# Kernel tuning notes

Hardware: AMD Instinct MI355X
Metric: run time of the kernel (lower is better)

Reference implementation:

```python
import jax, jax.numpy as jnp
import numpy as np

B, S, D, H = 4, 2048, 1024, 16
HD = D // H

def setup_inputs() -> dict:
    key = jax.random.key(0)
    ks = jax.random.split(key, 5)
    x = jax.random.normal(ks[0], (B, S, D), dtype=jnp.float32)
    mask = jnp.ones((B, S), dtype=jnp.int32)
    # torch nn.Linear init scale ~ 1/sqrt(fan_in); use small normal for stability
    qkv_w = jax.random.normal(ks[1], (3 * D, D), dtype=jnp.float32) * (1.0 / np.sqrt(D))
    qkv_b = jax.random.normal(ks[2], (3 * D,), dtype=jnp.float32) * 0.02
    out_w = jax.random.normal(ks[3], (D, D), dtype=jnp.float32) * (1.0 / np.sqrt(D))
    out_b = jax.random.normal(ks[4], (D,), dtype=jnp.float32) * 0.02
    return {"x": x, "mask": mask, "qkv_w": qkv_w, "qkv_b": qkv_b,
            "out_w": out_w, "out_b": out_b}

def reference(x, mask, qkv_w, qkv_b, out_w, out_b):
    b, s, d = x.shape
    scale = np.sqrt(HD).astype(np.float32)
    # qkv projection: torch Linear y = x @ W^T + b
    qkv = x @ qkv_w.T + qkv_b                      # (b, s, 3d)
    qkv = qkv.reshape(b, s, 3, H, HD)
    qkv = jnp.transpose(qkv, (2, 0, 3, 1, 4))      # (3, b, H, s, hd)
    q, k, v = qkv[0], qkv[1], qkv[2]
    scores = jnp.einsum('bhqd,bhkd->bhqk', q, k) / scale  # (b, H, s, s)
    neg_inf = jnp.float32(-jnp.inf)
    causal = jnp.tril(jnp.ones((s, s), dtype=bool))
    scores = jnp.where(causal[None, None], scores, neg_inf)
    key_mask = (mask != 0)[:, None, None, :]       # (b, 1, 1, s)
    scores = jnp.where(key_mask, scores, neg_inf)
    attn = jax.nn.softmax(scores, axis=-1)
    out = jnp.einsum('bhqk,bhkd->bhqd', attn, v)   # (b, H, s, hd)
    out = jnp.transpose(out, (0, 2, 1, 3)).reshape(b, s, d)
    return out @ out_w.T + out_b
```

## Files before the change

kernel.cpp:

```cpp
#include <hip/hip_runtime.h>
#include <stdint.h>
#include <type_traits>

#define BB  4
#define SS  2048
#define DD  1024
#define HH  16
#define HDD 64

typedef __attribute__((ext_vector_type(8)))  short s16x8;
typedef __attribute__((ext_vector_type(4)))  float f32x4;
typedef __attribute__((ext_vector_type(16))) float f32x16;

__device__ inline short f2bf(float f) {
    union { float f; unsigned int u; } v; v.f = f;
    unsigned int r = (v.u + 0x7fffu + ((v.u >> 16) & 1u)) >> 16;
    return (short)r;
}
__device__ inline unsigned int permpack(float a, float b) {
    union { float f; unsigned int u; } x, y; x.f = a; y.f = b;
    return __builtin_amdgcn_perm(y.u + 0x8000u, x.u + 0x8000u, 0x07060302u);
}

#define GLL(gp, lp) __builtin_amdgcn_global_load_lds( \
    (const __attribute__((address_space(1))) void*)(gp), \
    (__attribute__((address_space(3))) void*)(lp), 16, 0, 0)

__global__ void cvt_kernel(const float* __restrict__ src, short* __restrict__ dst, int n) {
    int i = (blockIdx.x * 256 + threadIdx.x) * 8;
    if (i >= n) return;
    const float4* s = (const float4*)(src + i);
    float4 a = s[0], b = s[1];
    s16x8 o;
    o[0]=f2bf(a.x); o[1]=f2bf(a.y); o[2]=f2bf(a.z); o[3]=f2bf(a.w);
    o[4]=f2bf(b.x); o[5]=f2bf(b.y); o[6]=f2bf(b.z); o[7]=f2bf(b.w);
    *(s16x8*)(dst + i) = o;
}

template<int EPI>
__global__ __launch_bounds__(256)
void gemm_bt(const short* __restrict__ A, const short* __restrict__ Bw,
             const float* __restrict__ bias, float* __restrict__ Cf,
             short* __restrict__ Qo, short* __restrict__ Ko, short* __restrict__ Vo,
             int M, int N, int K)
{
    __shared__ short lsA[128 * 32];
    __shared__ short lsB[128 * 32];
    const int tid  = threadIdx.x;
    const int w    = tid >> 6, lane = tid & 63;
    const int quad = lane >> 4, l15 = lane & 15;
    const int m0 = blockIdx.x * 128, n0 = blockIdx.y * 128;
    const int mw = (w & 1) * 64, nw = (w >> 1) * 64;

    f32x4 acc[4][4] = {};

    const int srow = w * 32 + (lane >> 2);
    const int scol = (lane & 3) * 8;
    const short* pA = A + (size_t)(m0 + srow) * K + scol;
    const short* pB = Bw + (size_t)(n0 + srow) * K + scol;
    short* lAbase0 = &lsA[(w * 32) * 32];
    short* lAbase1 = &lsA[(w * 32 + 16) * 32];
    short* lBbase0 = &lsB[(w * 32) * 32];
    short* lBbase1 = &lsB[(w * 32 + 16) * 32];

    for (int kk = 0; kk < K; kk += 32) {
        __syncthreads();
        GLL(pA + kk,            lAbase0);
        GLL(pA + kk + 16 * K,   lAbase1);
        GLL(pB + kk,            lBbase0);
        GLL(pB + kk + 16 * K,   lBbase1);
        asm volatile("s_waitcnt vmcnt(0)" ::: "memory");
        __syncthreads();

        s16x8 af[4], bfr[4];
        for (int t = 0; t < 4; ++t) {
            af[t]  = *(const s16x8*)&lsA[(mw + t * 16 + l15) * 32 + quad * 8];
            bfr[t] = *(const s16x8*)&lsB[(nw + t * 16 + l15) * 32 + quad * 8];
        }
        for (int i = 0; i < 4; ++i)
            for (int j = 0; j < 4; ++j)
                acc[i][j] = __builtin_amdgcn_mfma_f32_16x16x32_bf16(af[i], bfr[j], acc[i][j], 0, 0, 0);
    }

    if (EPI == 0) {
        for (int i = 0; i < 4; ++i) {
            int row = m0 + mw + i * 16 + quad * 4;
            for (int j = 0; j < 4; ++j) {
                int col = n0 + nw + j * 16 + l15;
                float bv = bias[col];
                for (int r = 0; r < 4; ++r)
                    Cf[(size_t)(row + r) * N + col] = acc[i][j][r] + bv;
            }
        }
    } else {
        for (int i = 0; i < 4; ++i) {
            int row = m0 + mw + i * 16 + quad * 4;
            for (int j = 0; j < 4; ++j) {
                int col = n0 + nw + j * 16 + l15;
                float bv = bias[col];
                int sel = col >> 10, h = (col >> 6) & 15, hd = col & 63;
                for (int r = 0; r < 4; ++r) {
                    int rr = row + r;
                    int b = rr >> 11, s = rr & 2047;
                    short val = f2bf(acc[i][j][r] + bv);
                    if (sel == 0)      Qo[(((size_t)b * HH + h) * SS + s) * HDD + hd] = val;
                    else if (sel == 1) Ko[(((size_t)b * HH + h) * SS + s) * HDD + hd] = val;
                    else               Vo[(((size_t)b * HH + h) * HDD + hd) * SS + s] = val;
                }
            }
        }
    }
}

__global__ __launch_bounds__(256, 4)
void attn_kernel(const short* __restrict__ Q, const short* __restrict__ Kb,
                 const short* __restrict__ Vb, const int* __restrict__ mask,
                 short* __restrict__ O)
{
    __shared__ short lsK[2][64 * 64];
    __shared__ short lsV[2][64 * 64];
    __shared__ float lsM[2][64];

    const int tid = threadIdx.x;
    const int w   = tid >> 6, lane = tid & 63;
    const int h   = lane >> 5, q = lane & 31;
    const int bx = blockIdx.x, bh = blockIdx.y;
    const int qb = (bx & 1) ? (15 - (bx >> 1)) : (bx >> 1);
    const int b = bh >> 4;
    const size_t baseQK = (size_t)bh * SS * HDD;
    const size_t baseV  = (size_t)bh * HDD * SS;
    const int q0 = qb * 128;
    const int s_row = q0 + w * 32 + q;
    const int T = 2 * (qb + 1);
    const float SC = 0.18033688f;

    s16x8 bq[4];
    for (int kb = 0; kb < 4; ++kb)
        bq[kb] = *(const s16x8*)(Q + baseQK + (size_t)s_row * HDD + kb * 16 + h * 8);

    const short* gK[2]; const short* gV[2]; int lofs[2];
    for (int i = 0; i < 2; ++i) {
        const int p = w * 128 + i * 64 + lane;
        const int kr = p >> 3, s = p & 7;
        gK[i] = Kb + baseQK + (size_t)kr * HDD + ((s ^ (kr & 7)) * 8);
        gV[i] = Vb + baseV + (size_t)kr * SS + ((s ^ (kr & 7)) * 8);
        lofs[i] = (w * 128 + i * 64) * 8;
    }
    const int* mbase = mask + b * SS;

    float lsum = 0.f;
    f32x16 oa[2] = {};

    for (int i = 0; i < 2; ++i) {
        GLL(gK[i], &lsK[0][lofs[i]]);
        GLL(gV[i], &lsV[0][lofs[i]]);
    }
    if (tid < 16) {
        int4 mv = *(const int4*)(mbase + tid * 4);
        float4 f;
        f.x = mv.x ? 0.f : -1e30f; f.y = mv.y ? 0.f : -1e30f;
        f.z = mv.z ? 0.f : -1e30f; f.w = mv.w ? 0.f : -1e30f;
        *(float4*)&lsM[0][tid * 4] = f;
    }
    __syncthreads();

    auto step = [&](int kt, auto CC) {
        constexpr bool CAUS = decltype(CC)::value;
        const int cur = kt & 1, nxt = cur ^ 1;
        const int kv0 = kt * 64;

        int4 mv;
        const bool pf = (kt + 1 < T);
        if (pf) {
            const size_t okK = (size_t)(kv0 + 64) * HDD;
            const int   okV = kv0 + 64;
            for (int i = 0; i < 2; ++i) {
                GLL(gK[i] + okK, &lsK[nxt][lofs[i]]);
                GLL(gV[i] + okV, &lsV[nxt][lofs[i]]);
            }
            if (tid < 16) mv = *(const int4*)(mbase + kv0 + 64 + tid * 4);
        }

        for (int nt = 0; nt < 2; ++nt) {
            f32x16 sa = {};
            const int key = nt * 32 + q;
            for (int kb = 0; kb < 4; ++kb) {
                const int cc = (kb * 2 + h) ^ (key & 7);
                s16x8 ak = *(const s16x8*)&lsK[cur][(key * 8 + cc) * 8];
                sa = __builtin_amdgcn_mfma_f32_32x32x16_bf16(ak, bq[kb], sa, 0, 0, 0);
            }
            unsigned int pk2[4][2];
            for (int g = 0; g < 4; ++g) {
                float4 mq = *(const float4*)&lsM[cur][nt * 32 + 8 * g + 4 * h];
                float pv[4];
                for (int r = 0; r < 4; ++r) {
                    float v = sa[g * 4 + r] * SC + ((const float*)&mq)[r];
                    if (CAUS) {
                        int keyg = kv0 + nt * 32 + 8 * g + 4 * h + r;
                        if (keyg > s_row) v = -1e30f;
                    }
                    float p = __builtin_amdgcn_exp2f(v);
                    pv[r] = p;
                    lsum += p;
                }
                pk2[g][0] = permpack(pv[0], pv[1]);
                pk2[g][1] = permpack(pv[2], pv[3]);
            }
            for (int kb2 = 0; kb2 < 2; ++kb2) {
                const int g_own = 2 * kb2 + h;
                unsigned int s0 = h ? pk2[2 * kb2][0] : pk2[2 * kb2 + 1][0];
                unsigned int s1 = h ? pk2[2 * kb2][1] : pk2[2 * kb2 + 1][1];
                unsigned int r0 = (unsigned int)__shfl_xor((int)s0, 32);
                unsigned int r1 = (unsigned int)__shfl_xor((int)s1, 32);
                union { s16x8 v; unsigned int d[4]; } bp;
                if (h == 0) { bp.d[0] = pk2[g_own][0]; bp.d[1] = pk2[g_own][1]; bp.d[2] = r0; bp.d[3] = r1; }
                else        { bp.d[0] = r0; bp.d[1] = r1; bp.d[2] = pk2[g_own][0]; bp.d[3] = pk2[g_own][1]; }
                for (int mt = 0; mt < 2; ++mt) {
                    const int hd = mt * 32 + q;
                    const int cc = (nt * 4 + kb2 * 2 + h) ^ (hd & 7);
                    s16x8 av = *(const s16x8*)&lsV[cur][(hd * 8 + cc) * 8];
                    oa[mt] = __builtin_amdgcn_mfma_f32_32x32x16_bf16(av, bp.v, oa[mt], 0, 0, 0);
                }
            }
        }

        if (pf && tid < 16) {
            float4 f;
            f.x = mv.x ? 0.f : -1e30f; f.y = mv.y ? 0.f : -1e30f;
            f.z = mv.z ? 0.f : -1e30f; f.w = mv.w ? 0.f : -1e30f;
            *(float4*)&lsM[nxt][tid * 4] = f;
        }
        __syncthreads();
    };

    int kt = 0;
    for (; kt < T - 2; ++kt) step(kt, std::false_type{});
    step(kt, std::true_type{}); ++kt;
    step(kt, std::true_type{});

    float ls2 = lsum + __shfl_xor(lsum, 32);
    float inv = 1.0f / ls2;
    const int hcol = (bh & 15) * HDD;
    const size_t obase = ((size_t)b * SS + s_row) * DD + hcol;
    for (int mt = 0; mt < 2; ++mt) {
        for (int g = 0; g < 4; ++g) {
            const int hd0 = mt * 32 + 8 * g + 4 * h;
            uint2 st;
            st.x = permpack(oa[mt][g * 4 + 0] * inv, oa[mt][g * 4 + 1] * inv);
            st.y = permpack(oa[mt][g * 4 + 2] * inv, oa[mt][g * 4 + 3] * inv);
            *(uint2*)&O[obase + hd0] = st;
        }
    }
}

extern "C" void kernel_launch(void* const* d_in, const int* in_sizes, int n_in,
                              void* d_out, int out_size, void* d_ws, size_t ws_size,
                              hipStream_t stream) {
    const float* x     = (const float*)d_in[0];
    const int*   mask  = (const int*)d_in[1];
    const float* qkv_w = (const float*)d_in[2];
    const float* qkv_b = (const float*)d_in[3];
    const float* out_w = (const float*)d_in[4];
    const float* out_b = (const float*)d_in[5];
    float* out = (float*)d_out;

    const size_t M1 = (size_t)BB * SS;
    short* ws  = (short*)d_ws;
    short* xb  = ws;
    short* qwb = xb  + M1 * DD;
    short* owb = qwb + (size_t)3 * DD * DD;
    short* Qb  = owb + (size_t)DD * DD;
    short* Kb  = Qb  + M1 * DD;
    short* Vb  = Kb  + M1 * DD;
    short* Ob  = Vb  + M1 * DD;

    cvt_kernel<<<(int)(M1 * DD / 8 / 256), 256, 0, stream>>>(x, xb, (int)(M1 * DD));
    cvt_kernel<<<3 * DD * DD / 8 / 256, 256, 0, stream>>>(qkv_w, qwb, 3 * DD * DD);
    cvt_kernel<<<DD * DD / 8 / 256, 256, 0, stream>>>(out_w, owb, DD * DD);

    gemm_bt<1><<<dim3(64, 24), 256, 0, stream>>>(xb, qwb, qkv_b, nullptr,
                                                 Qb, Kb, Vb, 8192, 3072, 1024);
    attn_kernel<<<dim3(16, BB * HH), 256, 0, stream>>>(Qb, Kb, Vb, mask, Ob);
    gemm_bt<0><<<dim3(64, 8), 256, 0, stream>>>(Ob, owb, out_b, out,
                                                nullptr, nullptr, nullptr, 8192, 1024, 1024);
}
```

Measured before the change: 341.3 us.

## Split attention work across warps by key half and head-dim half per 32-query block

Each attention block now handles only 32 query rows instead of 128. Its four waves split the 64-key tile into two key halves and the head dimension into two halves, and the partial outputs and row sums are combined through shared memory at the end. The grid grows from 16 to 64 blocks per head, with descending query-block order, to improve load balance and occupancy under the causal mask. In exchange, each wave now computes QK^T scores that its partner wave duplicates for the other head-dim half. K/V tiles are also loaded once per 32 queries rather than once per 128, which adds global and LDS traffic.

```diff
diff --git a/kernel.cpp b/kernel.cpp
--- a/kernel.cpp
+++ b/kernel.cpp
@@ -124,14 +124,14 @@
     const int tid = threadIdx.x;
     const int w   = tid >> 6, lane = tid & 63;
     const int h   = lane >> 5, q = lane & 31;
+    const int kh  = w & 1, hdh = w >> 1;
     const int bx = blockIdx.x, bh = blockIdx.y;
-    const int qb = (bx & 1) ? (15 - (bx >> 1)) : (bx >> 1);
+    const int qs = 63 - bx;
     const int b = bh >> 4;
     const size_t baseQK = (size_t)bh * SS * HDD;
     const size_t baseV  = (size_t)bh * HDD * SS;
-    const int q0 = qb * 128;
-    const int s_row = q0 + w * 32 + q;
-    const int T = 2 * (qb + 1);
+    const int s_row = qs * 32 + q;
+    const int T = (qs >> 1) + 1;
     const float SC = 0.18033688f;
 
     s16x8 bq[4];
@@ -141,15 +141,15 @@
     const short* gK[2]; const short* gV[2]; int lofs[2];
     for (int i = 0; i < 2; ++i) {
         const int p = w * 128 + i * 64 + lane;
-        const int kr = p >> 3, s = p & 7;
-        gK[i] = Kb + baseQK + (size_t)kr * HDD + ((s ^ (kr & 7)) * 8);
-        gV[i] = Vb + baseV + (size_t)kr * SS + ((s ^ (kr & 7)) * 8);
+        const int kr = p >> 3, sc = p & 7;
+        gK[i] = Kb + baseQK + (size_t)kr * HDD + ((sc ^ (kr & 7)) * 8);
+        gV[i] = Vb + baseV + (size_t)kr * SS + ((sc ^ (kr & 7)) * 8);
         lofs[i] = (w * 128 + i * 64) * 8;
     }
     const int* mbase = mask + b * SS;
 
     float lsum = 0.f;
-    f32x16 oa[2] = {};
+    f32x16 oa = {};
 
     for (int i = 0; i < 2; ++i) {
         GLL(gK[i], &lsK[0][lofs[i]]);
@@ -181,47 +181,43 @@
             if (tid < 16) mv = *(const int4*)(mbase + kv0 + 64 + tid * 4);
         }
 
-        for (int nt = 0; nt < 2; ++nt) {
-            f32x16 sa = {};
-            const int key = nt * 32 + q;
-            for (int kb = 0; kb < 4; ++kb) {
-                const int cc = (kb * 2 + h) ^ (key & 7);
-                s16x8 ak = *(const s16x8*)&lsK[cur][(key * 8 + cc) * 8];
-                sa = __builtin_amdgcn_mfma_f32_32x32x16_bf16(ak, bq[kb], sa, 0, 0, 0);
-            }
-            unsigned int pk2[4][2];
-            for (int g = 0; g < 4; ++g) {
-                float4 mq = *(const float4*)&lsM[cur][nt * 32 + 8 * g + 4 * h];
-                float pv[4];
-                for (int r = 0; r < 4; ++r) {
-                    float v = sa[g * 4 + r] * SC + ((const float*)&mq)[r];
-                    if (CAUS) {
-                        int keyg = kv0 + nt * 32 + 8 * g + 4 * h + r;
-                        if (keyg > s_row) v = -1e30f;
-                    }
-                    float p = __builtin_amdgcn_exp2f(v);
-                    pv[r] = p;
-                    lsum += p;
+        f32x16 sa = {};
+        const int keyl = kh * 32 + q;
+        for (int kb = 0; kb < 4; ++kb) {
+            const int cc = (kb * 2 + h) ^ (keyl & 7);
+            s16x8 ak = *(const s16x8*)&lsK[cur][(keyl * 8 + cc) * 8];
+            sa = __builtin_amdgcn_mfma_f32_32x32x16_bf16(ak, bq[kb], sa, 0, 0, 0);
+        }
+        unsigned int pk2[4][2];
+        for (int g = 0; g < 4; ++g) {
+            float4 mq = *(const float4*)&lsM[cur][kh * 32 + 8 * g + 4 * h];
+            float pv[4];
+            for (int r = 0; r < 4; ++r) {
+                float v = sa[g * 4 + r] * SC + ((const float*)&mq)[r];
+                if (CAUS) {
+                    int keyg = kv0 + kh * 32 + 8 * g + 4 * h + r;
+                    if (keyg > s_row) v = -1e30f;
                 }
-                pk2[g][0] = permpack(pv[0], pv[1]);
-                pk2[g][1] = permpack(pv[2], pv[3]);
-            }
-            for (int kb2 = 0; kb2 < 2; ++kb2) {
-                const int g_own = 2 * kb2 + h;
-                unsigned int s0 = h ? pk2[2 * kb2][0] : pk2[2 * kb2 + 1][0];
-                unsigned int s1 = h ? pk2[2 * kb2][1] : pk2[2 * kb2 + 1][1];
-                unsigned int r0 = (unsigned int)__shfl_xor((int)s0, 32);
-                unsigned int r1 = (unsigned int)__shfl_xor((int)s1, 32);
-                union { s16x8 v; unsigned int d[4]; } bp;
-                if (h == 0) { bp.d[0] = pk2[g_own][0]; bp.d[1] = pk2[g_own][1]; bp.d[2] = r0; bp.d[3] = r1; }
-                else        { bp.d[0] = r0; bp.d[1] = r1; bp.d[2] = pk2[g_own][0]; bp.d[3] = pk2[g_own][1]; }
-                for (int mt = 0; mt < 2; ++mt) {
-                    const int hd = mt * 32 + q;
-                    const int cc = (nt * 4 + kb2 * 2 + h) ^ (hd & 7);
-                    s16x8 av = *(const s16x8*)&lsV[cur][(hd * 8 + cc) * 8];
-                    oa[mt] = __builtin_amdgcn_mfma_f32_32x32x16_bf16(av, bp.v, oa[mt], 0, 0, 0);
-                }
-            }
+                float p = __builtin_amdgcn_exp2f(v);
+                pv[r] = p;
+                lsum += p;
+            }
+            pk2[g][0] = permpack(pv[0], pv[1]);
+            pk2[g][1] = permpack(pv[2], pv[3]);
+        }
+        for (int kb2 = 0; kb2 < 2; ++kb2) {
+            const int g_own = 2 * kb2 + h;
+            unsigned int s0 = h ? pk2[2 * kb2][0] : pk2[2 * kb2 + 1][0];
+            unsigned int s1 = h ? pk2[2 * kb2][1] : pk2[2 * kb2 + 1][1];
+            unsigned int r0 = (unsigned int)__shfl_xor((int)s0, 32);
+            unsigned int r1 = (unsigned int)__shfl_xor((int)s1, 32);
+            union { s16x8 v; unsigned int d[4]; } bp;
+            if (h == 0) { bp.d[0] = pk2[g_own][0]; bp.d[1] = pk2[g_own][1]; bp.d[2] = r0; bp.d[3] = r1; }
+            else        { bp.d[0] = r0; bp.d[1] = r1; bp.d[2] = pk2[g_own][0]; bp.d[3] = pk2[g_own][1]; }
+            const int hd = hdh * 32 + q;
+            const int cc = (kh * 4 + kb2 * 2 + h) ^ (hd & 7);
+            s16x8 av = *(const s16x8*)&lsV[cur][(hd * 8 + cc) * 8];
+            oa = __builtin_amdgcn_mfma_f32_32x32x16_bf16(av, bp.v, oa, 0, 0, 0);
         }
 
         if (pf && tid < 16) {
@@ -233,21 +229,30 @@
         __syncthreads();
     };
 
-    int kt = 0;
-    for (; kt < T - 2; ++kt) step(kt, std::false_type{});
-    step(kt, std::true_type{}); ++kt;
-    step(kt, std::true_type{});
+    for (int kt = 0; kt < T - 1; ++kt) step(kt, std::false_type{});
+    step(T - 1, std::true_type{});
 
     float ls2 = lsum + __shfl_xor(lsum, 32);
-    float inv = 1.0f / ls2;
-    const int hcol = (bh & 15) * HDD;
-    const size_t obase = ((size_t)b * SS + s_row) * DD + hcol;
-    for (int mt = 0; mt < 2; ++mt) {
+    float* cmb = (float*)&lsK[0][0];
+    float* cls = (float*)&lsV[0][0];
+    if (kh == 1) {
+        *(f32x16*)(cmb + hdh * 1024 + lane * 16) = oa;
+        cls[hdh * 64 + lane] = ls2;
+    }
+    __syncthreads();
+    if (kh == 0) {
+        f32x16 po = *(const f32x16*)(cmb + hdh * 1024 + lane * 16);
+        float lt = ls2 + cls[hdh * 64 + lane];
+        float inv = 1.0f / lt;
+        const int hcol = (bh & 15) * HDD;
+        const size_t obase = ((size_t)b * SS + s_row) * DD + hcol;
         for (int g = 0; g < 4; ++g) {
-            const int hd0 = mt * 32 + 8 * g + 4 * h;
+            const int hd0 = hdh * 32 + 8 * g + 4 * h;
             uint2 st;
-            st.x = permpack(oa[mt][g * 4 + 0] * inv, oa[mt][g * 4 + 1] * inv);
-            st.y = permpack(oa[mt][g * 4 + 2] * inv, oa[mt][g * 4 + 3] * inv);
+            st.x = permpack((oa[g * 4 + 0] + po[g * 4 + 0]) * inv,
+                            (oa[g * 4 + 1] + po[g * 4 + 1]) * inv);
+            st.y = permpack((oa[g * 4 + 2] + po[g * 4 + 2]) * inv,
+                            (oa[g * 4 + 3] + po[g * 4 + 3]) * inv);
             *(uint2*)&O[obase + hd0] = st;
         }
     }
@@ -280,7 +285,7 @@
 
     gemm_bt<1><<<dim3(64, 24), 256, 0, stream>>>(xb, qwb, qkv_b, nullptr,
                                                  Qb, Kb, Vb, 8192, 3072, 1024);
-    attn_kernel<<<dim3(16, BB * HH), 256, 0, stream>>>(Qb, Kb, Vb, mask, Ob);
+    attn_kernel<<<dim3(64, BB * HH), 256, 0, stream>>>(Qb, Kb, Vb, mask, Ob);
     gemm_bt<0><<<dim3(64, 8), 256, 0, stream>>>(Ob, owb, out_b, out,
                                                 nullptr, nullptr, nullptr, 8192, 1024, 1024);
 }
```

After: 376.8 us. 10.4% more time.
